# Performance work log

Hardware: AMD Instinct MI355X
Metric: run time of the kernel (lower is better)

Reference implementation:

```python
import jax, jax.numpy as jnp
import numpy as np

EPS = 1e-15

def gcn_sparse(x, row, col, ew, W, b, n):
    # PyG GCNConv: h = x@W; add self-loops (weight 1); sym-normalize; aggregate at col (target); + bias
    h = x @ W
    loop = jnp.arange(n)
    r = jnp.concatenate([row, loop])
    c = jnp.concatenate([col, loop])
    w = jnp.concatenate([ew, jnp.ones((n,), x.dtype)])
    deg = jax.ops.segment_sum(w, c, num_segments=n)
    dinv = jnp.where(deg > 0, deg ** -0.5, 0.0)
    norm = dinv[r] * w * dinv[c]
    out = jax.ops.segment_sum(norm[:, None] * h[r], c, num_segments=n)
    return out + b

def gcn_dense(x, adj, W, b):
    # Dense equivalent of dense_to_sparse + GCNConv: existing nonzero self-loops keep their
    # weight, zero-diagonal nodes get a self-loop of weight 1 (add_remaining_self_loops).
    diag = jnp.diagonal(adj)
    adj_h = adj + jnp.diag(jnp.where(diag == 0, 1.0, 0.0).astype(adj.dtype))
    deg = adj_h.sum(axis=0)  # degree at target (col) nodes
    dinv = jnp.where(deg > 0, deg ** -0.5, 0.0)
    a_norm = dinv[:, None] * adj_h * dinv[None, :]  # norm_ij = d_i^-1/2 a_ij d_j^-1/2
    return a_norm.T @ (x @ W) + b  # out_j = sum_i norm_ij h_i

def diff_pool(x, adj, s, mask=None):
    s = jax.nn.softmax(s, axis=-1)
    if mask is not None:
        x = x * mask[:, None]
        s = s * mask[:, None]
    out = s.T @ x                      # [C, F]
    out_adj = s.T @ (adj @ s)          # [C, C]
    link = jnp.linalg.norm(adj - s @ s.T) / adj.size
    ent = jnp.mean(jnp.sum(-s * jnp.log(s + EPS), axis=-1))
    return out, out_adj, link, ent

def setup_inputs() -> dict:
    N, E, F, H, C1, C2, NC = 8192, 262144, 128, 128, 1024, 128, 16
    key = jax.random.key(0)
    ks = jax.random.split(key, 16)
    x0 = jax.random.normal(ks[0], (N, F), dtype=jnp.float32)
    edge_index = jax.random.randint(ks[1], (2, E), 0, N, dtype=jnp.int32)
    edge_weight = jax.random.uniform(ks[2], (E,), dtype=jnp.float32)
    adj = jnp.zeros((N, N), jnp.float32).at[edge_index[0], edge_index[1]].add(edge_weight)
    mask = jnp.ones((N,), jnp.float32)
    g = lambda k, i, o: jax.random.normal(k, (i, o), dtype=jnp.float32) * (1.0 / np.sqrt(i))
    return {
        'x0': x0, 'edge_index': edge_index, 'edge_weight': edge_weight,
        'adj': adj, 'mask': mask,
        'W0_in': g(ks[3], F, H),      'b0_in': jnp.zeros((H,)),
        'Wp1':   g(ks[4], H, C1),     'bp1':   jnp.zeros((C1,)),
        'W1_in': g(ks[5], H, H),      'b1_in': jnp.zeros((H,)),
        'Wp2':   g(ks[6], H, C2),     'bp2':   jnp.zeros((C2,)),
        'W2_in': g(ks[7], H, H),      'b2_in': jnp.zeros((H,)),
        'W1_out': g(ks[8], 2 * H, H), 'b1_out': jnp.zeros((H,)),
        'W0_out': g(ks[9], 2 * H, NC), 'b0_out': jnp.zeros((NC,)),
    }

def reference(x0, edge_index, edge_weight, adj, mask,
              W0_in, b0_in, Wp1, bp1, W1_in, b1_in, Wp2, bp2,
              W2_in, b2_in, W1_out, b1_out, W0_out, b0_out):
    n = x0.shape[0]
    row, col = edge_index[0], edge_index[1]
    x0_ = jax.nn.relu(gcn_sparse(x0, row, col, edge_weight, W0_in, b0_in, n))
    s1 = jax.nn.relu(gcn_sparse(x0_, row, col, edge_weight, Wp1, bp1, n))
    x1, adj1, l1, e1 = diff_pool(x0_, adj, s1, mask)
    x1_ = jax.nn.relu(gcn_dense(x1, adj1, W1_in, b1_in))
    s2 = jax.nn.relu(gcn_dense(x1_, adj1, Wp2, bp2))
    x2, adj2, l2, e2 = diff_pool(x1_, adj1, s2)
    x2_out = jax.nn.relu(gcn_dense(x2, adj2, W2_in, b2_in))
    x2_out_up = s2 @ x2_out  # unpool with pre-softmax relu s2, as in source
    x1_out = jax.nn.relu(gcn_dense(jnp.concatenate([x1_, x2_out_up], axis=1), adj1, W1_out, b1_out))
    x1_out_up = s1 @ x1_out
    x0_out = jax.nn.relu(gcn_sparse(jnp.concatenate([x0_, x1_out_up], axis=1), row, col, edge_weight, W0_out, b0_out, n))
    prediction = jax.nn.log_softmax(x0_out, axis=1)
    edge_loss = l1 + e1 + l2 + e2
    return prediction, s1, edge_loss, adj1
```

## Files before the change

kernel.cpp:

```cpp
#include <hip/hip_runtime.h>
#include <math.h>


#define N_NODES 8192
#define N_EDGES 262144

typedef __attribute__((ext_vector_type(8))) short short8;
typedef __attribute__((ext_vector_type(4))) float floatx4;

#define OFF_DEG     0
#define OFF_CNTC    8192
#define OFF_CNTR    16384
#define OFF_SCAL    24576
#define ZERO_FLOATS 24592
#define OFF_COLPTR  24592
#define OFF_ROWPTR  32785
#define OFF_CURC    40978
#define OFF_CURR    49170
#define OFF_COLR    57362
#define OFF_COLN    319506
#define OFF_ROWC    581650
#define OFF_ROWW    843794
#define OFF_DINV    1105938
#define OFF_X0      1114144
#define OFF_H0      2162720
#define OFF_S       3211296
#define OFF_AN1TB   OFF_S
#define OFF_ADJ1B   (OFF_S+524288)
#define OFF_HAT     (OFF_S+1048576)
#define OFF_HBT     (OFF_S+1114112)
#define OFF_HCATT   (OFF_S+1179648)
#define OFF_S2ST    (OFF_S+1245184)
#define OFF_X0T     7405600
#define OFF_X0B     7929888
#define A2          8454176
#define OFF_X1      (A2+0)
#define OFF_Y16     (A2+131072)
#define OFF_X1_     (A2+262144)
#define OFF_S2      (A2+524288)
#define OFF_S2S     (A2+655360)
#define OFF_U       (A2+786432)
#define OFF_X2      (A2+917504)
#define OFF_ADJ2    (A2+933888)
#define OFF_HC      (A2+950272)
#define OFF_X2_     (A2+966656)
#define OFF_Z2      (A2+999424)
#define OFF_X1O     (A2+1261568)
#define OFF_P16     (A2+1392640)
#define OFF_DI1     (A2+1654784)
#define OFF_DF1     (A2+1655808)
#define OFF_DI2     (A2+1656832)
#define OFF_DF2     (A2+1656960)
#define OFF_ST      10111264
#define OFF_TBF     14305568
#define OFF_WP1T    OFF_TBF
#define OFF_PADJ    OFF_TBF
#define OFF_PG      22694176
#define OFF_PP      OFF_PG
#define OFF_PX1     31082784
#define OFF_TT2     32131360

#define OUT_PRED 0
#define OUT_S1   131072
#define OUT_LOSS 8519680
#define OUT_ADJ1 8519681

__device__ __forceinline__ unsigned short f2bf(float f) {
    union { float f; unsigned u; } v; v.f = f;
    unsigned r = (v.u + 0x7FFF + ((v.u >> 16) & 1)) >> 16;
    return (unsigned short)r;
}
__device__ __forceinline__ float bf2f(unsigned short b) {
    union { unsigned u; float f; } v; v.u = (unsigned)b << 16; return v.f;
}
__device__ __forceinline__ void gl_lds16(const unsigned short* g, unsigned short* l) {
    __builtin_amdgcn_global_load_lds(
        (const __attribute__((address_space(1))) void*)g,
        (__attribute__((address_space(3))) void*)l, 16, 0, 0);
}


__global__ void k_hist(const int* __restrict__ row, const int* __restrict__ col,
                       const float* __restrict__ ew, int E,
                       float* deg, int* cntc, int* cntr, float* sumA2) {
    __shared__ float red[256];
    int e = blockIdx.x * 256 + threadIdx.x;
    float w2 = 0.f;
    if (e < E) {
        int r = row[e], c = col[e];
        float w = ew[e];
        atomicAdd(&deg[c], w);
        atomicAdd(&cntc[c], 1);
        atomicAdd(&cntr[r], 1);
        w2 = w * w;
    }
    red[threadIdx.x] = w2; __syncthreads();
    for (int s = 128; s > 0; s >>= 1) { if (threadIdx.x < s) red[threadIdx.x] += red[threadIdx.x + s]; __syncthreads(); }
    if (threadIdx.x == 0) atomicAdd(sumA2, red[0]);
}

__global__ __launch_bounds__(1024) void k_scan(const int* cntc, const int* cntr,
        int* colptr, int* rowptr, int* curc, int* curr, int n, int E,
        const float* __restrict__ deg, float* __restrict__ dinv) {
    __shared__ int part[1024];
    int tid = threadIdx.x;
    const int per = 8;
    for (int pass = 0; pass < 2; ++pass) {
        const int* cnt = pass ? cntr : cntc;
        int* ptr = pass ? rowptr : colptr;
        int* cur = pass ? curr : curc;
        int st = tid * per;
        int loc[per]; int s = 0;
        for (int i = 0; i < per; ++i) { loc[i] = s; s += cnt[st + i]; }
        part[tid] = s; __syncthreads();
        for (int off = 1; off < 1024; off <<= 1) {
            int v = part[tid];
            int add = (tid >= off) ? part[tid - off] : 0;
            __syncthreads();
            part[tid] = v + add;
            __syncthreads();
        }
        int pre = (tid == 0) ? 0 : part[tid - 1];
        for (int i = 0; i < per; ++i) { int v = pre + loc[i]; ptr[st + i] = v; cur[st + i] = v; }
        if (tid == 0) ptr[n] = E;
        __syncthreads();
    }
    for (int i = tid; i < n; i += 1024) {
        float d = deg[i] + 1.0f;
        dinv[i] = (d > 0.f) ? 1.0f / sqrtf(d) : 0.f;
    }
}

__global__ void k_scatter(const int* __restrict__ row, const int* __restrict__ col,
                          const float* __restrict__ ew, int E, const float* __restrict__ dinv,
                          int* curc, int* curr, int* colr, float* coln, int* rowc, float* roww) {
    int e = blockIdx.x * 256 + threadIdx.x;
    if (e >= E) return;
    int r = row[e], c = col[e];
    float w = ew[e];
    float nrm = dinv[r] * w * dinv[c];
    int p = atomicAdd(&curc[c], 1);
    colr[p] = r; coln[p] = nrm;
// ... 227 lines not shown
            float a0 = As[ty * 2][kk], a1 = As[ty * 2 + 1][kk];
            float b0 = Bs[kk][tx * 2], b1 = Bs[kk][tx * 2 + 1];
            acc[0][0] += a0 * b0; acc[0][1] += a0 * b1;
            acc[1][0] += a1 * b0; acc[1][1] += a1 * b1;
        }
        __syncthreads();
    }
    if (op == 2) {
        float ss = acc[0][0] * acc[0][0] + acc[0][1] * acc[0][1]
                 + acc[1][0] * acc[1][0] + acc[1][1] * acc[1][1];
        red[tid] = ss; __syncthreads();
        for (int s = 128; s > 0; s >>= 1) { if (tid < s) red[tid] += red[tid + s]; __syncthreads(); }
        if (tid == 0) atomicAdd(ss_acc, red[0]);
        return;
    }
    float* C = (op == 0) ? C0 : C1;
    #pragma unroll
    for (int i = 0; i < 2; ++i)
        #pragma unroll
        for (int j = 0; j < 2; ++j)
            C[(size_t)(m0 + ty * 2 + i) * N + n0 + tx * 2 + j] = acc[i][j];
}

__global__ __launch_bounds__(256) void k_gemm_n16(const float* __restrict__ A, const float* __restrict__ B,
        float* __restrict__ C, int M, int K, int accum) {
    __shared__ float As[16][64];
    __shared__ float Bs[64][16];
    int tid = threadIdx.x;
    int r = tid >> 4, c = tid & 15;
    int m0 = blockIdx.x * 16;
    float acc = 0.f;
    for (int k0 = 0; k0 < K; k0 += 64) {
        #pragma unroll
        for (int l = 0; l < 4; ++l) {
            int idx = tid + 256 * l;
            int rr = idx >> 6, cc = idx & 63;
            As[rr][cc] = A[(size_t)(m0 + rr) * K + k0 + cc];
            int kk = idx >> 4, c2 = idx & 15;
            Bs[kk][c2] = B[(size_t)(k0 + kk) * 16 + c2];
        }
        __syncthreads();
        #pragma unroll 16
        for (int kk = 0; kk < 64; ++kk) acc += As[r][kk] * Bs[kk][c];
        __syncthreads();
    }
    float* p = &C[(size_t)(m0 + r) * 16 + c];
    if (accum) acc += *p;
    *p = acc;
}

__global__ __launch_bounds__(256) void k_gemm_n16_dual(
        const float* __restrict__ A0, int K0, const float* __restrict__ B0,
        const float* __restrict__ A1, int K1, const float* __restrict__ B1,
        float* __restrict__ C, int M) {
    __shared__ float As[16][64];
    __shared__ float Bs[64][16];
    int tid = threadIdx.x;
    int r = tid >> 4, c = tid & 15;
    int m0 = blockIdx.x * 16;
    float acc = 0.f;
    for (int src = 0; src < 2; ++src) {
        const float* A = src ? A1 : A0;
        const float* B = src ? B1 : B0;
        int K = src ? K1 : K0;
        for (int k0 = 0; k0 < K; k0 += 64) {
            #pragma unroll
            for (int l = 0; l < 4; ++l) {
                int idx = tid + 256 * l;
                int rr = idx >> 6, cc = idx & 63;
                As[rr][cc] = A[(size_t)(m0 + rr) * K + k0 + cc];
                int kk = idx >> 4, c2 = idx & 15;
                Bs[kk][c2] = B[(size_t)(k0 + kk) * 16 + c2];
            }
            __syncthreads();
            #pragma unroll 16
            for (int kk = 0; kk < 64; ++kk) acc += As[r][kk] * Bs[kk][c];
            __syncthreads();
        }
    }
    C[(size_t)(m0 + r) * 16 + c] = acc;
}


__global__ __launch_bounds__(256) void gemm_tn_bf16_part(
        const unsigned short* __restrict__ A, const unsigned short* __restrict__ B,
        float* __restrict__ P, int M, int N, int K) {
    __shared__ __align__(16) unsigned short As[128 * 64];
    __shared__ __align__(16) unsigned short Bs[128 * 64];
    int tid = threadIdx.x;
    int wave = tid >> 6, lane = tid & 63;
    int wm = wave >> 1, wn = wave & 1;
    int m0 = blockIdx.x * 128, n0 = blockIdx.y * 128;
    int kchunk = K / gridDim.z;
    int k0 = blockIdx.z * kchunk;
    float* Pz = P + (size_t)blockIdx.z * M * N;
    floatx4 acc[4][4] = {};
    int q = lane >> 4, lm = lane & 15;
    int lrow = lane >> 3, lcol = (lane & 7) * 8;
    for (int kt = 0; kt < kchunk; kt += 64) {
        int gk0 = k0 + kt;
        #pragma unroll
        for (int p = 0; p < 4; ++p) {
            int rbase = wave * 32 + p * 8;
            int row = rbase + lrow;
            int scol = lcol ^ ((row & 7) * 8);
            gl_lds16(&A[(size_t)(m0 + row) * K + gk0 + scol], &As[rbase * 64]);
            gl_lds16(&B[(size_t)(n0 + row) * K + gk0 + scol], &Bs[rbase * 64]);
        }
        __syncthreads();
        #pragma unroll
        for (int ks = 0; ks < 64; ks += 32) {
            short8 af[4], bf[4];
            int kk = ks + q * 8;
            #pragma unroll
            for (int i = 0; i < 4; ++i) {
                int ml = wm * 64 + i * 16 + lm;
                af[i] = *(const short8*)(&As[ml * 64 + (kk ^ ((ml & 7) * 8))]);
                int nl = wn * 64 + i * 16 + lm;
                bf[i] = *(const short8*)(&Bs[nl * 64 + (kk ^ ((nl & 7) * 8))]);
            }
            #pragma unroll
            for (int i = 0; i < 4; ++i)
                #pragma unroll
                for (int j = 0; j < 4; ++j)
                    acc[i][j] = __builtin_amdgcn_mfma_f32_16x16x32_bf16(af[i], bf[j], acc[i][j], 0, 0, 0);
        }
        __syncthreads();
    }
    for (int i = 0; i < 4; ++i) {
        int rowb = m0 + wm * 64 + i * 16 + q * 4;
        for (int j = 0; j < 4; ++j) {
            int col = n0 + wn * 64 + j * 16 + lm;
            #pragma unroll
            for (int r = 0; r < 4; ++r)
                Pz[(size_t)(rowb + r) * N + col] = acc[i][j][r];
        }
    }
}

__global__ __launch_bounds__(256) void gemm_tn_bf16_part3(
        const unsigned short* __restrict__ A,
        const unsigned short* __restrict__ B0, const unsigned short* __restrict__ B1,
        const unsigned short* __restrict__ B2,
        float* __restrict__ P0, float* __restrict__ P1, float* __restrict__ P2,
        int K) {
    __shared__ __align__(16) unsigned short As[128 * 64];
    __shared__ __align__(16) unsigned short Bs[128 * 64];
    int tid = threadIdx.x;
    int wave = tid >> 6, lane = tid & 63;
    int wm = wave >> 1, wn = wave & 1;
    int by = blockIdx.y;
    const unsigned short* B; float* P; int N, n0;
    if (by < 8)       { B = B0; P = P0; N = 1024; n0 = by * 128; }
    else if (by < 16) { B = B1; P = P1; N = 1024; n0 = (by - 8) * 128; }
    else              { B = B2; P = P2; N = 128;  n0 = 0; }
    int m0 = blockIdx.x * 128;
    int kchunk = K / gridDim.z;
    int k0 = blockIdx.z * kchunk;
    float* Pz = P + (size_t)blockIdx.z * 1024 * N;
    floatx4 acc[4][4] = {};
    int q = lane >> 4, lm = lane & 15;
    int lrow = lane >> 3, lcol = (lane & 7) * 8;
    for (int kt = 0; kt < kchunk; kt += 64) {
        int gk0 = k0 + kt;
        #pragma unroll
        for (int p = 0; p < 4; ++p) {
            int rbase = wave * 32 + p * 8;
            int row = rbase + lrow;
            int scol = lcol ^ ((row & 7) * 8);
            gl_lds16(&A[(size_t)(m0 + row) * K + gk0 + scol], &As[rbase * 64]);
            gl_lds16(&B[(size_t)(n0 + row) * K + gk0 + scol], &Bs[rbase * 64]);
        }
        __syncthreads();
        #pragma unroll
        for (int ks = 0; ks < 64; ks += 32) {
            short8 af[4], bf[4];
            int kk = ks + q * 8;
            #pragma unroll
            for (int i = 0; i < 4; ++i) {
                int ml = wm * 64 + i * 16 + lm;
                af[i] = *(const short8*)(&As[ml * 64 + (kk ^ ((ml & 7) * 8))]);
                int nl = wn * 64 + i * 16 + lm;
                bf[i] = *(const short8*)(&Bs[nl * 64 + (kk ^ ((nl & 7) * 8))]);
            }
            #pragma unroll
            for (int i = 0; i < 4; ++i)
                #pragma unroll
                for (int j = 0; j < 4; ++j)
                    acc[i][j] = __builtin_amdgcn_mfma_f32_16x16x32_bf16(af[i], bf[j], acc[i][j], 0, 0, 0);
        }
        __syncthreads();
    }
    for (int i = 0; i < 4; ++i) {
        int rowb = m0 + wm * 64 + i * 16 + q * 4;
        for (int j = 0; j < 4; ++j) {
            int col = n0 + wn * 64 + j * 16 + lm;
            #pragma unroll
            for (int r = 0; r < 4; ++r)
                Pz[(size_t)(rowb + r) * N + col] = acc[i][j][r];
        }
    }
}

__global__ __launch_bounds__(256) void gemm_tn_bf16_store(
        const unsigned short* __restrict__ A, const unsigned short* __restrict__ B,
        float* __restrict__ C, int M, int N, int K,
        const float* __restrict__ bias, int relu) {
    __shared__ __align__(16) unsigned short As[128 * 64];
    __shared__ __align__(16) unsigned short Bs[128 * 64];
    int tid = threadIdx.x;
    int wave = tid >> 6, lane = tid & 63;
    int wm = wave >> 1, wn = wave & 1;
    int m0 = blockIdx.x * 128, n0 = blockIdx.y * 128;
    floatx4 acc[4][4] = {};
    int q = lane >> 4, lm = lane & 15;
    int lrow = lane >> 3, lcol = (lane & 7) * 8;
    for (int kt = 0; kt < K; kt += 64) {
        #pragma unroll
        for (int p = 0; p < 4; ++p) {
            int rbase = wave * 32 + p * 8;
            int row = rbase + lrow;
            int scol = lcol ^ ((row & 7) * 8);
            gl_lds16(&A[(size_t)(m0 + row) * K + kt + scol], &As[rbase * 64]);
            gl_lds16(&B[(size_t)(n0 + row) * K + kt + scol], &Bs[rbase * 64]);
        }
        __syncthreads();
        #pragma unroll
        for (int ks = 0; ks < 64; ks += 32) {
            short8 af[4], bf[4];
            int kk = ks + q * 8;
            #pragma unroll
            for (int i = 0; i < 4; ++i) {
                int ml = wm * 64 + i * 16 + lm;
                af[i] = *(const short8*)(&As[ml * 64 + (kk ^ ((ml & 7) * 8))]);
                int nl = wn * 64 + i * 16 + lm;
                bf[i] = *(const short8*)(&Bs[nl * 64 + (kk ^ ((nl & 7) * 8))]);
            }
            #pragma unroll
            for (int i = 0; i < 4; ++i)
                #pragma unroll
                for (int j = 0; j < 4; ++j)
                    acc[i][j] = __builtin_amdgcn_mfma_f32_16x16x32_bf16(af[i], bf[j], acc[i][j], 0, 0, 0);
        }
        __syncthreads();
    }
    for (int i = 0; i < 4; ++i) {
        int rowb = m0 + wm * 64 + i * 16 + q * 4;
        for (int j = 0; j < 4; ++j) {
            int col = n0 + wn * 64 + j * 16 + lm;
            float bv = bias ? bias[col] : 0.f;
            #pragma unroll
            for (int r = 0; r < 4; ++r) {
                float v = acc[i][j][r] + bv;
                if (relu) v = fmaxf(v, 0.f);
                C[(size_t)(rowb + r) * N + col] = v;
            }
        }
    }
}

__global__ __launch_bounds__(256) void k_reduce3m(
        const float* __restrict__ P0, float* __restrict__ C0, unsigned short* __restrict__ Cb0, float* ss0,
        const float* __restrict__ P1, float* ss1,
        const float* __restrict__ P2, float* __restrict__ C2) {
    __shared__ float red[256];
    const float* P; float* C; unsigned short* Cb; float* ss; int n;
    if (blockIdx.y == 0)      { P = P0; C = C0;      Cb = Cb0;     ss = ss0;     n = 1024 * 1024; }
    else if (blockIdx.y == 1) { P = P1; C = nullptr; Cb = nullptr; ss = ss1;     n = 1024 * 1024; }
    else                      { P = P2; C = C2;      Cb = nullptr; ss = nullptr; n = 1024 * 128; }
    float ssv = 0.f;
    for (int i4 = (blockIdx.x * 256 + threadIdx.x) * 4; i4 < n; i4 += gridDim.x * 256 * 4) {
        float4 v = *(const float4*)(P + i4);
        #pragma unroll
        for (int s = 1; s < 8; ++s) {
            float4 w = *(const float4*)(P + (size_t)s * n + i4);
            v.x += w.x; v.y += w.y; v.z += w.z; v.w += w.w;
        }
        if (C) *(float4*)(C + i4) = v;
        if (Cb) {
            ushort4 o; o.x = f2bf(v.x); o.y = f2bf(v.y); o.z = f2bf(v.z); o.w = f2bf(v.w);
            *(ushort4*)(Cb + i4) = o;
        }
        ssv += v.x * v.x + v.y * v.y + v.z * v.z + v.w * v.w;
    }
    if (!ss) return;
    red[threadIdx.x] = ssv; __syncthreads();
    for (int s = 128; s > 0; s >>= 1) { if (threadIdx.x < s) red[threadIdx.x] += red[threadIdx.x + s]; __syncthreads(); }
    if (threadIdx.x == 0) atomicAdd(ss, red[0]);
}

__global__ __launch_bounds__(256) void k_reduce_br(const float* __restrict__ P,
        float* __restrict__ C, int n, int N, int nsplit,
        const float* __restrict__ bias, int relu) {
    for (int i4 = (blockIdx.x * 256 + threadIdx.x) * 4; i4 < n; i4 += gridDim.x * 256 * 4) {
        float4 v = *(const float4*)(P + i4);
        for (int s = 1; s < nsplit; ++s) {
            float4 w = *(const float4*)(P + (size_t)s * n + i4);
            v.x += w.x; v.y += w.y; v.z += w.z; v.w += w.w;
        }
        if (bias) {
            float4 b = *(const float4*)(bias + (i4 % N));
            v.x += b.x; v.y += b.y; v.z += b.z; v.w += b.w;
        }
        if (relu) {
            v.x = fmaxf(v.x, 0.f); v.y = fmaxf(v.y, 0.f);
            v.z = fmaxf(v.z, 0.f); v.w = fmaxf(v.w, 0.f);
        }
        *(float4*)(C + i4) = v;
    }
}


__global__ __launch_bounds__(256) void k_transpose_f2b(
        const float* __restrict__ in, unsigned short* __restrict__ outb,
        int R, int C, const float* __restrict__ rowscale) {
    __shared__ float tile[64][65];
    int rb = blockIdx.y * 64, cb = blockIdx.x * 64;
    int t = threadIdx.x;
    int lr = t >> 4, lc4 = (t & 15) * 4;
    #pragma unroll
    for (int p = 0; p < 4; ++p) {
        int r = rb + lr + p * 16;
        float4 v = *(const float4*)(in + (size_t)r * C + cb + lc4);
        float s = rowscale ? rowscale[r] : 1.0f;
        tile[lr + p * 16][lc4 + 0] = v.x * s;
        tile[lr + p * 16][lc4 + 1] = v.y * s;
        tile[lr + p * 16][lc4 + 2] = v.z * s;
        tile[lr + p * 16][lc4 + 3] = v.w * s;
    }
    __syncthreads();
    int cc0 = t >> 5, rr = (t & 31) * 2;
    #pragma unroll
    for (int p = 0; p < 8; ++p) {
        int cc = cc0 + p * 8;
        unsigned a = f2bf(tile[rr][cc]);
        unsigned b = f2bf(tile[rr + 1][cc]);
        *(unsigned*)(outb + (size_t)(cb + cc) * R + rb + rr) = a | (b << 16);
    }
}

__global__ __launch_bounds__(256) void k_transpose_b2b2(
        const unsigned short* __restrict__ in0, unsigned short* __restrict__ out0,
        const unsigned short* __restrict__ in1, unsigned short* __restrict__ out1,
        int R, int C) {
    __shared__ __align__(16) unsigned short tile[64][72];
    const unsigned short* in = blockIdx.z ? in1 : in0;
    unsigned short* out = blockIdx.z ? out1 : out0;
    int rb = blockIdx.y * 64, cb = blockIdx.x * 64;
    int t = threadIdx.x;
    int lr = t >> 3, lc = (t & 7) * 8;
    #pragma unroll
    for (int p = 0; p < 2; ++p) {
        int r = lr + p * 32;
        *(short8*)(&tile[r][lc]) = *(const short8*)(&in[(size_t)(rb + r) * C + cb + lc]);
    }
    __syncthreads();
    int cc0 = t >> 4, rr = (t & 15) * 4;
    #pragma unroll
    for (int p = 0; p < 4; ++p) {
        int cc = cc0 + p * 16;
        unsigned long long v = (unsigned long long)tile[rr][cc]
                             | ((unsigned long long)tile[rr + 1][cc] << 16)
                             | ((unsigned long long)tile[rr + 2][cc] << 32)
                             | ((unsigned long long)tile[rr + 3][cc] << 48);
        *(unsigned long long*)(&out[(size_t)(cb + cc) * R + rb + rr]) = v;
    }
}

__global__ __launch_bounds__(256) void k_anorm_tb(const float* __restrict__ adjm, int n,
        const float* __restrict__ dinvv, const float* __restrict__ dfix,
        unsigned short* __restrict__ outb) {
    __shared__ float tile[64][65];
    int rb = blockIdx.y * 64, cb = blockIdx.x * 64;
    int t = threadIdx.x;
    int lr = t >> 4, lc4 = (t & 15) * 4;
    #pragma unroll
    for (int p = 0; p < 4; ++p) {
        int i = rb + lr + p * 16;
        float4 v = *(const float4*)(adjm + (size_t)i * n + cb + lc4);
        float di = dinvv[i];
        float vv[4] = {v.x, v.y, v.z, v.w};
        #pragma unroll
        for (int q = 0; q < 4; ++q) {
            int j = cb + lc4 + q;
            float val = vv[q];
            if (i == j) val += dfix[i];
            tile[lr + p * 16][lc4 + q] = di * val * dinvv[j];
        }
    }
    __syncthreads();
    int cc0 = t >> 5, rr = (t & 31) * 2;
// ... 92 lines not shown
    m = red[0]; __syncthreads();
    float e0 = expf(v.x - m), e1 = expf(v.y - m), e2 = expf(v.z - m), e3 = expf(v.w - m);
    red[tid] = e0 + e1 + e2 + e3; __syncthreads();
    for (int s = 128; s > 0; s >>= 1) { if (tid < s) red[tid] += red[tid + s]; __syncthreads(); }
    float inv = 1.0f / red[0]; __syncthreads();
    float mk = mask ? mask[r] : 1.0f;
    float s0 = e0 * inv * mk, s1 = e1 * inv * mk, s2 = e2 * inv * mk, s3 = e3 * inv * mk;
    float ent = -(s0 * logf(s0 + 1e-15f) + s1 * logf(s1 + 1e-15f)
                + s2 * logf(s2 + 1e-15f) + s3 * logf(s3 + 1e-15f));
    ushort4 o;
    o.x = f2bf(s0); o.y = f2bf(s1); o.z = f2bf(s2); o.w = f2bf(s3);
    *(ushort4*)(Sb + (size_t)r * 1024 + tid * 4) = o;
    red[tid] = ent; __syncthreads();
    for (int s = 128; s > 0; s >>= 1) { if (tid < s) red[tid] += red[tid + s]; __syncthreads(); }
    if (tid == 0) atomicAdd(ent_acc, red[0]);
}

__global__ __launch_bounds__(256) void k_softmax_ent(const float* __restrict__ x, float* __restrict__ S,
        int W, const float* __restrict__ mask, float* ent_acc) {
    __shared__ float red[256];
    int row = blockIdx.x, tid = threadIdx.x;
    const float* xr = x + (size_t)row * W;
    float m = -3.0e38f;
    for (int q = tid; q < W; q += 256) m = fmaxf(m, xr[q]);
    red[tid] = m; __syncthreads();
    for (int s = 128; s > 0; s >>= 1) { if (tid < s) red[tid] = fmaxf(red[tid], red[tid + s]); __syncthreads(); }
    m = red[0]; __syncthreads();
    float sum = 0.f;
    for (int q = tid; q < W; q += 256) sum += expf(xr[q] - m);
    red[tid] = sum; __syncthreads();
    for (int s = 128; s > 0; s >>= 1) { if (tid < s) red[tid] += red[tid + s]; __syncthreads(); }
    float inv = 1.0f / red[0]; __syncthreads();
    float mk = mask ? mask[row] : 1.0f;
    float* Sr = S + (size_t)row * W;
    float ent = 0.f;
    for (int q = tid; q < W; q += 256) {
        float v = expf(xr[q] - m) * inv * mk;
        Sr[q] = v;
        ent -= v * logf(v + 1e-15f);
    }
    red[tid] = ent; __syncthreads();
    for (int s = 128; s > 0; s >>= 1) { if (tid < s) red[tid] += red[tid + s]; __syncthreads(); }
    if (tid == 0) atomicAdd(ent_acc, red[0]);
}

__global__ __launch_bounds__(256) void k_spmm_seg(const unsigned short* __restrict__ Sb,
        const int* __restrict__ rptr, const int* __restrict__ rowc, const float* __restrict__ roww,
        unsigned short* __restrict__ tb) {
    int wave = threadIdx.x >> 6, lane = threadIdx.x & 63;
    int r = blockIdx.x * 4 + wave;
    int j0 = blockIdx.y * 256 + lane * 4;
    const unsigned short* Sj = Sb + j0;
    float a0 = 0.f, a1 = 0.f, a2 = 0.f, a3 = 0.f;
    int e0 = rptr[r], e1 = rptr[r + 1];
    int e = e0;
    for (; e + 4 <= e1; e += 4) {
        int c0 = rowc[e], c1 = rowc[e + 1], c2 = rowc[e + 2], c3 = rowc[e + 3];
        float w0 = roww[e], w1 = roww[e + 1], w2 = roww[e + 2], w3 = roww[e + 3];
        uint2 v0 = *(const uint2*)(Sj + (size_t)c0 * 1024);
        uint2 v1 = *(const uint2*)(Sj + (size_t)c1 * 1024);
        uint2 v2 = *(const uint2*)(Sj + (size_t)c2 * 1024);
        uint2 v3 = *(const uint2*)(Sj + (size_t)c3 * 1024);
        a0 += w0 * bf2f((unsigned short)(v0.x & 0xffff)) + w1 * bf2f((unsigned short)(v1.x & 0xffff))
            + w2 * bf2f((unsigned short)(v2.x & 0xffff)) + w3 * bf2f((unsigned short)(v3.x & 0xffff));
        a1 += w0 * bf2f((unsigned short)(v0.x >> 16)) + w1 * bf2f((unsigned short)(v1.x >> 16))
            + w2 * bf2f((unsigned short)(v2.x >> 16)) + w3 * bf2f((unsigned short)(v3.x >> 16));
        a2 += w0 * bf2f((unsigned short)(v0.y & 0xffff)) + w1 * bf2f((unsigned short)(v1.y & 0xffff))
            + w2 * bf2f((unsigned short)(v2.y & 0xffff)) + w3 * bf2f((unsigned short)(v3.y & 0xffff));
        a3 += w0 * bf2f((unsigned short)(v0.y >> 16)) + w1 * bf2f((unsigned short)(v1.y >> 16))
            + w2 * bf2f((unsigned short)(v2.y >> 16)) + w3 * bf2f((unsigned short)(v3.y >> 16));
    }
    for (; e < e1; ++e) {
        int c = rowc[e]; float w = roww[e];
        uint2 v = *(const uint2*)(Sj + (size_t)c * 1024);
        a0 += w * bf2f((unsigned short)(v.x & 0xffff));
        a1 += w * bf2f((unsigned short)(v.x >> 16));
        a2 += w * bf2f((unsigned short)(v.y & 0xffff));
        a3 += w * bf2f((unsigned short)(v.y >> 16));
    }
    unsigned lo = (unsigned)f2bf(a0) | ((unsigned)f2bf(a1) << 16);
    unsigned hi = (unsigned)f2bf(a2) | ((unsigned)f2bf(a3) << 16);
    unsigned long long o = (unsigned long long)lo | ((unsigned long long)hi << 32);
    *(unsigned long long*)(tb + (size_t)r * 1024 + j0) = o;
}

__global__ __launch_bounds__(256) void k_coldfix1024(const float* __restrict__ adjm,
        float* dinvv, float* dfix, float* cross_acc) {
    __shared__ float part[4][64];
    __shared__ float red[256];
    int jl = threadIdx.x & 63;
    int j = blockIdx.x * 64 + jl;
    int rg = threadIdx.x >> 6;
    float s = 0.f;
    for (int r = rg * 256; r < rg * 256 + 256; ++r)
        s += adjm[(size_t)r * 1024 + j];
    part[rg][jl] = s;
    __syncthreads();
    float diag = 0.f;
    if (rg == 0) {
        float tot = part[0][jl] + part[1][jl] + part[2][jl] + part[3][jl];
        diag = adjm[(size_t)j * 1024 + j];
        float fix = (diag == 0.f) ? 1.0f : 0.f;
        tot += fix;
        dfix[j] = fix;
        dinvv[j] = (tot > 0.f) ? 1.0f / sqrtf(tot) : 0.f;
    }
    red[threadIdx.x] = diag; __syncthreads();
    for (int st = 128; st > 0; st >>= 1) { if (threadIdx.x < st) red[threadIdx.x] += red[threadIdx.x + st]; __syncthreads(); }
    if (threadIdx.x == 0) atomicAdd(cross_acc, red[0]);
}

__global__ __launch_bounds__(128) void k_coldfix128(const float* __restrict__ adjm,
        float* dinvv, float* dfix, float* cross2_out) {
    __shared__ float red[128];
    int j = threadIdx.x;
    float s = 0.f;
    for (int i = 0; i < 128; ++i) s += adjm[(size_t)i * 128 + j];
    float diag = adjm[(size_t)j * 128 + j];
    float fix = (diag == 0.f) ? 1.0f : 0.f;
    s += fix;
    dfix[j] = fix;
    dinvv[j] = (s > 0.f) ? 1.0f / sqrtf(s) : 0.f;
    red[j] = diag; __syncthreads();
    for (int st = 64; st > 0; st >>= 1) { if (j < st) red[j] += red[j + st]; __syncthreads(); }
    if (j == 0) *cross2_out = red[0];
}

__global__ void k_finalize(const float* __restrict__ sc, float* loss) {
    if (threadIdx.x == 0 && blockIdx.x == 0) {
        float e1     = sc[0] / 8192.0f;
        float cross  = sc[1];
        float g2     = sc[2];
        float sumA2  = sc[3];
        float ssadj1 = sc[4];
        float e2     = sc[5] / 1024.0f;
        float cross2 = sc[6];
        float g2b    = sc[7];
        float l1 = sqrtf(fmaxf(sumA2 - 2.0f * cross + g2, 0.f)) / 67108864.0f;
        float l2 = sqrtf(fmaxf(ssadj1 - 2.0f * cross2 + g2b, 0.f)) / 1048576.0f;
        *loss = l1 + e1 + l2 + e2;
    }
}


extern "C" void kernel_launch(void* const* d_in, const int* in_sizes, int n_in,
                              void* d_out, int out_size, void* d_ws, size_t ws_size,
                              hipStream_t stream) {
    const int N = N_NODES, E = N_EDGES;
    const float* x0     = (const float*)d_in[0];
    const int*   eidx   = (const int*)d_in[1];
    const float* ew     = (const float*)d_in[2];
    const float* mask   = (const float*)d_in[4];
    const float* W0_in  = (const float*)d_in[5];
    const float* b0_in  = (const float*)d_in[6];
    const float* Wp1    = (const float*)d_in[7];
    const float* bp1    = (const float*)d_in[8];
    const float* W1_in  = (const float*)d_in[9];
    const float* b1_in  = (const float*)d_in[10];
    const float* Wp2    = (const float*)d_in[11];
    const float* bp2    = (const float*)d_in[12];
    const float* W2_in  = (const float*)d_in[13];
    const float* b2_in  = (const float*)d_in[14];
    const float* W1_out = (const float*)d_in[15];
    const float* b1_out = (const float*)d_in[16];
    const float* W0_out = (const float*)d_in[17];
    const float* b0_out = (const float*)d_in[18];

    float* out   = (float*)d_out;
    float* predo = out + OUT_PRED;
    float* s1o   = out + OUT_S1;
    float* losso = out + OUT_LOSS;
    float* adj1o = out + OUT_ADJ1;

    float* wsf = (float*)d_ws;
    int*   wsi = (int*)d_ws;
    float* deg   = wsf + OFF_DEG;
    int*   cntc  = wsi + OFF_CNTC;
    int*   cntr  = wsi + OFF_CNTR;
    float* scal  = wsf + OFF_SCAL;
    int*   cptr  = wsi + OFF_COLPTR;
    int*   rptr  = wsi + OFF_ROWPTR;
    int*   curc  = wsi + OFF_CURC;
    int*   curr  = wsi + OFF_CURR;
    int*   colr  = wsi + OFF_COLR;
    float* coln  = wsf + OFF_COLN;
    int*   rowc  = wsi + OFF_ROWC;
    float* roww  = wsf + OFF_ROWW;
    float* dinv  = wsf + OFF_DINV;
    float* x0_   = wsf + OFF_X0;
    unsigned short* h0b   = (unsigned short*)(wsf + OFF_H0);
    unsigned short* Sb    = (unsigned short*)(wsf + OFF_S);
    unsigned short* TT    = (unsigned short*)(wsf + OFF_TT2);
    unsigned short* AN1TB = (unsigned short*)(wsf + OFF_AN1TB);
    unsigned short* ADJ1B = (unsigned short*)(wsf + OFF_ADJ1B);
    unsigned short* HAT   = (unsigned short*)(wsf + OFF_HAT);
    unsigned short* HBT   = (unsigned short*)(wsf + OFF_HBT);
    unsigned short* HCATT = (unsigned short*)(wsf + OFF_HCATT);
    unsigned short* S2ST  = (unsigned short*)(wsf + OFF_S2ST);
    unsigned short* ST    = (unsigned short*)(wsf + OFF_ST);
    unsigned short* TBF   = (unsigned short*)(wsf + OFF_TBF);
    unsigned short* WP1T  = (unsigned short*)(wsf + OFF_WP1T);
    unsigned short* X0T   = (unsigned short*)(wsf + OFF_X0T);
    unsigned short* x0b   = (unsigned short*)(wsf + OFF_X0B);
    float* PADJ  = wsf + OFF_PADJ;
    float* PG    = wsf + OFF_PG;
    float* PP    = wsf + OFF_PP;
    float* PX1   = wsf + OFF_PX1;
    float* x1    = wsf + OFF_X1;
    float* y16   = wsf + OFF_Y16;
    float* x1_   = wsf + OFF_X1_;
    float* s2    = wsf + OFF_S2;
    float* S2s   = wsf + OFF_S2S;
    float* u     = wsf + OFF_U;
    float* x2    = wsf + OFF_X2;
    float* adj2  = wsf + OFF_ADJ2;
    float* hC    = wsf + OFF_HC;
    float* x2_   = wsf + OFF_X2_;
    float* z2    = wsf + OFF_Z2;
    float* x1o_  = wsf + OFF_X1O;
    float* p16   = wsf + OFF_P16;
    float* di1   = wsf + OFF_DI1;
    float* df1   = wsf + OFF_DF1;
    float* di2   = wsf + OFF_DI2;
    float* df2   = wsf + OFF_DF2;

    const int* row = eidx;
    const int* col = eidx + E;

    hipMemsetAsync(wsf, 0, (size_t)ZERO_FLOATS * sizeof(float), stream);

    k_hist<<<E / 256, 256, 0, stream>>>(row, col, ew, E, deg, cntc, cntr, &scal[3]);
    k_scan<<<1, 1024, 0, stream>>>(cntc, cntr, cptr, rptr, curc, curr, N, E, deg, dinv);
    k_scatter<<<E / 256, 256, 0, stream>>>(row, col, ew, E, dinv, curc, curr, colr, coln, rowc, roww);

    gemm_ab_b16<<<dim3(2, 128), 256, 0, stream>>>(x0, W0_in, h0b, 8192, 128, 128);
    k_agg_b16<<<N, 64, 0, stream>>>(h0b, x0_, x0b, cptr, colr, coln, dinv, b0_in, 1);

    k_agg_b16<<<N, 64, 0, stream>>>(x0b, nullptr, h0b, cptr, colr, coln, dinv, nullptr, 0);
    k_transpose_f2b<<<dim3(16, 2), 256, 0, stream>>>(Wp1, WP1T, 128, 1024, nullptr);
    gemm_tn_bf16_store<<<dim3(64, 8), 256, 0, stream>>>(h0b, WP1T, s1o, 8192, 1024, 128, bp1, 1);

    k_softmax1024<<<N, 256, 0, stream>>>(s1o, Sb, mask, &scal[0]);
    k_spmm_seg<<<dim3(N / 4, 4), 256, 0, stream>>>(Sb, rptr, rowc, roww, TBF);
    k_transpose_b2b2<<<dim3(16, 128, 2), 256, 0, stream>>>(Sb, ST, TBF, TT, 8192, 1024);
    k_transpose_f2b<<<dim3(2, 128), 256, 0, stream>>>(x0_, X0T, 8192, 128, mask);

    gemm_tn_bf16_part3<<<dim3(8, 17, 8), 256, 0, stream>>>(ST, TT, ST, X0T, PADJ, PG, PX1, 8192);
    k_reduce3m<<<dim3(1024, 3), 256, 0, stream>>>(PADJ, adj1o, ADJ1B, &scal[4], PG, &scal[2], PX1, x1);

    k_coldfix1024<<<16, 256, 0, stream>>>(adj1o, di1, df1, &scal[1]);
    k_anorm_tb<<<dim3(16, 16), 256, 0, stream>>>(adj1o, 1024, di1, df1, AN1TB);

    gemm_ab32_bt<<<dim3(4, 32), 256, 0, stream>>>(x1, W1_in, HAT, 1024, 128, 128);
    gemm_tn_bf16_part<<<dim3(8, 1, 16), 256, 0, stream>>>(AN1TB, HAT, PP, 1024, 128, 1024);
    k_reduce_br<<<128, 256, 0, stream>>>(PP, x1_, 1024 * 128, 128, 16, b1_in, 1);
    gemm_ab32_bt<<<dim3(4, 32), 256, 0, stream>>>(x1_, Wp2, HBT, 1024, 128, 128);
    gemm_tn_bf16_part<<<dim3(8, 1, 16), 256, 0, stream>>>(AN1TB, HBT, PP, 1024, 128, 1024);
    k_reduce_br<<<128, 256, 0, stream>>>(PP, s2, 1024 * 128, 128, 16, bp2, 1);

    k_softmax_ent<<<1024, 256, 0, stream>>>(s2, S2s, 128, nullptr, &scal[5]);
    k_transpose_f2b<<<dim3(2, 16), 256, 0, stream>>>(S2s, S2ST, 1024, 128, nullptr);
    gemm_tn_bf16_part<<<dim3(8, 1, 16), 256, 0, stream>>>(ADJ1B, S2ST, PP, 1024, 128, 1024);
    k_reduce_br<<<128, 256, 0, stream>>>(PP, u, 1024 * 128, 128, 16, nullptr, 0);
    k_atb32_3<<<dim3(4, 4, 3), 256, 0, stream>>>(S2s, x1_, u, S2s, x2, adj2, &scal[7], 128, 128, 1024);

    k_coldfix128<<<1, 128, 0, stream>>>(adj2, di2, df2, &scal[6]);
    gemm_ab32<<<dim3(4, 4), 256, 0, stream>>>(x2, W2_in, hC, 128, 128, 128, nullptr, 0, 0);
    gemm_atb32n<<<dim3(4, 4), 256, 0, stream>>>(adj2, hC, x2_, 128, 128, 128, b2_in, di2, df2, di2);

    gemm_ab32<<<dim3(4, 4), 256, 0, stream>>>(x2_, W1_out + 128 * 128, z2, 128, 128, 128, nullptr, 0, 0);
    gemm_dual_bt<<<dim3(4, 32), 256, 0, stream>>>(x1_, W1_out, s2, z2, HCATT, 1024, 128, 128);
    gemm_tn_bf16_part<<<dim3(8, 1, 16), 256, 0, stream>>>(AN1TB, HCATT, PP, 1024, 128, 1024);
    k_reduce_br<<<128, 256, 0, stream>>>(PP, x1o_, 1024 * 128, 128, 16, b1_out, 1);

    k_gemm_n16<<<64, 256, 0, stream>>>(x1o_, W0_out + 128 * 16, y16, 1024, 128, 0);
    k_gemm_n16_dual<<<512, 256, 0, stream>>>(x0_, 128, W0_out, s1o, 1024, y16, p16, 8192);
    k_agg16_ls<<<512, 256, 0, stream>>>(p16, predo, cptr, colr, coln, dinv, b0_out);

    k_finalize<<<1, 64, 0, stream>>>(scal, losso);
}
```

Before: 945.8 us.

## Exploit S^T S symmetry, cut split-K, and drop partial-sum reductions for small GEMMs

The big pooling GEMM now computes only the upper-triangular tiles of S^T S, which is needed only for the link-loss norm, and counts off-diagonal tiles twice. Split-K drops from 8 to 4 to shrink the partial buffers. A new reduction kernel fuses the column degree, diagonal and trace computation, replacing the column-sum kernel that re-read adj1. The 1024x128 dense GEMMs switch to a non-split 64x64-tile kernel with fused bias and ReLU, which removes the 16-way partial-sum writes and the separate reduction launches. The cost is fewer blocks (32) for the small GEMMs, with a full K=1024 loop per block, and atomic accumulation for the degrees.

After: 895.2 us. -5.4%, faster.

```diff
diff --git a/kernel.cpp b/kernel.cpp
--- a/kernel.cpp
+++ b/kernel.cpp
@@ -47,6 +47,8 @@
 #define OFF_Z2      (A2+999424)
 #define OFF_X1O     (A2+1261568)
 #define OFF_P16     (A2+1392640)
+#define OFF_DEG1    OFF_P16
+#define OFF_DIAGV   (OFF_P16+1024)
 #define OFF_DI1     (A2+1654784)
 #define OFF_DF1     (A2+1655808)
 #define OFF_DI2     (A2+1656832)
@@ -54,10 +56,7 @@
 #define OFF_ST      10111264
 #define OFF_TBF     14305568
 #define OFF_WP1T    OFF_TBF
-#define OFF_PADJ    OFF_TBF
-#define OFF_PG      22694176
-#define OFF_PP      OFF_PG
-#define OFF_PX1     31082784
+#define OFF_PT      OFF_TBF
 #define OFF_TT2     32131360
 
 #define OUT_PRED 0
@@ -451,18 +450,27 @@
 }
 
 
-__global__ __launch_bounds__(256) void gemm_tn_bf16_part(
-        const unsigned short* __restrict__ A, const unsigned short* __restrict__ B,
-        float* __restrict__ P, int M, int N, int K) {
+__global__ __launch_bounds__(256) void gemm_tn_bf16_tiles(
+        const unsigned short* __restrict__ ST_,
+        const unsigned short* __restrict__ TT_,
+        const unsigned short* __restrict__ X0T_,
+        float* __restrict__ P, int K) {
     __shared__ __align__(16) unsigned short As[128 * 64];
     __shared__ __align__(16) unsigned short Bs[128 * 64];
     int tid = threadIdx.x;
     int wave = tid >> 6, lane = tid & 63;
     int wm = wave >> 1, wn = wave & 1;
-    int m0 = blockIdx.x * 128, n0 = blockIdx.y * 128;
-    int kchunk = K / gridDim.z;
-    int k0 = blockIdx.z * kchunk;
-    float* Pz = P + (size_t)blockIdx.z * M * N;
+    int tile = blockIdx.x;
+    int m, n; const unsigned short* B;
+    if (tile < 64)       { m = tile >> 3; n = tile & 7; B = TT_; }
+    else if (tile < 100) { int p = tile - 64; int ti = 0;
+                           while (p >= 8 - ti) { p -= 8 - ti; ++ti; }
+                           m = ti; n = ti + p; B = ST_; }
+    else                 { m = tile - 100; n = 0; B = X0T_; }
+    int m0 = m * 128, n0 = n * 128;
+    int kchunk = K / gridDim.y;
+    int k0 = blockIdx.y * kchunk;
+    float* Pz = P + ((size_t)blockIdx.y * 108 + tile) * 16384;
     floatx4 acc[4][4] = {};
     int q = lane >> 4, lm = lane & 15;
     int lrow = lane >> 3, lcol = (lane & 7) * 8;
@@ -473,7 +481,7 @@
             int rbase = wave * 32 + p * 8;
             int row = rbase + lrow;
             int scol = lcol ^ ((row & 7) * 8);
-            gl_lds16(&A[(size_t)(m0 + row) * K + gk0 + scol], &As[rbase * 64]);
+            gl_lds16(&ST_[(size_t)(m0 + row) * K + gk0 + scol], &As[rbase * 64]);
             gl_lds16(&B[(size_t)(n0 + row) * K + gk0 + scol], &Bs[rbase * 64]);
         }
         __syncthreads();
@@ -497,76 +505,146 @@
         __syncthreads();
     }
     for (int i = 0; i < 4; ++i) {
-        int rowb = m0 + wm * 64 + i * 16 + q * 4;
+        int lr = wm * 64 + i * 16 + q * 4;
         for (int j = 0; j < 4; ++j) {
-            int col = n0 + wn * 64 + j * 16 + lm;
+            int lc = wn * 64 + j * 16 + lm;
             #pragma unroll
             for (int r = 0; r < 4; ++r)
-                Pz[(size_t)(rowb + r) * N + col] = acc[i][j][r];
-        }
-    }
-}
-
-__global__ __launch_bounds__(256) void gemm_tn_bf16_part3(
-        const unsigned short* __restrict__ A,
-        const unsigned short* __restrict__ B0, const unsigned short* __restrict__ B1,
-        const unsigned short* __restrict__ B2,
-        float* __restrict__ P0, float* __restrict__ P1, float* __restrict__ P2,
-        int K) {
-    __shared__ __align__(16) unsigned short As[128 * 64];
-    __shared__ __align__(16) unsigned short Bs[128 * 64];
-    int tid = threadIdx.x;
-    int wave = tid >> 6, lane = tid & 63;
-    int wm = wave >> 1, wn = wave & 1;
-    int by = blockIdx.y;
-    const unsigned short* B; float* P; int N, n0;
-    if (by < 8)       { B = B0; P = P0; N = 1024; n0 = by * 128; }
-    else if (by < 16) { B = B1; P = P1; N = 1024; n0 = (by - 8) * 128; }
-    else              { B = B2; P = P2; N = 128;  n0 = 0; }
-    int m0 = blockIdx.x * 128;
-    int kchunk = K / gridDim.z;
-    int k0 = blockIdx.z * kchunk;
-    float* Pz = P + (size_t)blockIdx.z * 1024 * N;
-    floatx4 acc[4][4] = {};
+                Pz[(size_t)(lr + r) * 128 + lc] = acc[i][j][r];
+        }
+    }
+}
+
+__global__ __launch_bounds__(256) void k_reduce_tiles(
+        const float* __restrict__ P,
+        float* __restrict__ adj1o, unsigned short* __restrict__ adj1b,
+        float* __restrict__ x1, float* __restrict__ deg1, float* __restrict__ diagv,
+        float* __restrict__ scal) {
+    __shared__ float colsum[128];
+    __shared__ float red[256];
+    int tile = blockIdx.y, half = blockIdx.x, tid = threadIdx.x;
+    if (tid < 128) colsum[tid] = 0.f;
+    __syncthreads();
+    int m, n, kind;
+    if (tile < 64)       { kind = 0; m = tile >> 3; n = tile & 7; }
+    else if (tile < 100) { kind = 1; int p = tile - 64; int ti = 0;
+                           while (p >= 8 - ti) { p -= 8 - ti; ++ti; }
+                           m = ti; n = ti + p; }
+    else                 { kind = 2; m = tile - 100; n = 0; }
+    const float* Pt = P + (size_t)tile * 16384 + half * 8192;
+    const size_t zstr = (size_t)108 * 16384;
+    float ss = 0.f, tr = 0.f;
+    float cs0 = 0.f, cs1 = 0.f, cs2 = 0.f, cs3 = 0.f;
+    int cc = (tid * 4) & 127;
+    bool diagTile = (kind == 0) && (m == n);
+    float wgt = (kind == 1 && m != n) ? 2.f : 1.f;
+    for (int it = 0; it < 8; ++it) {
+        int i4 = tid * 4 + it * 1024;
+        float4 v = *(const float4*)(Pt + i4);
+        #pragma unroll
+        for (int z = 1; z < 4; ++z) {
+            float4 w4 = *(const float4*)(Pt + zstr * z + i4);
+            v.x += w4.x; v.y += w4.y; v.z += w4.z; v.w += w4.w;
+        }
+        int rr = i4 >> 7;
+        if (kind == 0) {
+            size_t gaddr = (size_t)(m * 128 + half * 64 + rr) * 1024 + n * 128 + cc;
+            *(float4*)(adj1o + gaddr) = v;
+            ushort4 o; o.x = f2bf(v.x); o.y = f2bf(v.y); o.z = f2bf(v.z); o.w = f2bf(v.w);
+            *(ushort4*)(adj1b + gaddr) = o;
+            cs0 += v.x; cs1 += v.y; cs2 += v.z; cs3 += v.w;
+            ss += v.x * v.x + v.y * v.y + v.z * v.z + v.w * v.w;
+            if (diagTile) {
+                int dloc = half * 64 + rr;
+                int dj = dloc - cc;
+                if (dj >= 0 && dj < 4) {
+                    float dv = (dj == 0) ? v.x : (dj == 1) ? v.y : (dj == 2) ? v.z : v.w;
+                    diagv[m * 128 + dloc] = dv;
+                    tr += dv;
+                }
+            }
+        } else if (kind == 1) {
+            ss += wgt * (v.x * v.x + v.y * v.y + v.z * v.z + v.w * v.w);
+        } else {
+            *(float4*)(x1 + (size_t)(m * 128 + half * 64) * 128 + i4) = v;
+        }
+    }
+    if (kind == 2) return;
+    if (kind == 0) {
+        atomicAdd(&colsum[cc + 0], cs0);
+        atomicAdd(&colsum[cc + 1], cs1);
+        atomicAdd(&colsum[cc + 2], cs2);
+        atomicAdd(&colsum[cc + 3], cs3);
+    }
+    __syncthreads();
+    if (kind == 0 && tid < 128)
+        atomicAdd(&deg1[n * 128 + tid], colsum[tid]);
+    red[tid] = ss; __syncthreads();
+    for (int s = 128; s > 0; s >>= 1) { if (tid < s) red[tid] += red[tid + s]; __syncthreads(); }
+    if (tid == 0) atomicAdd((kind == 0) ? &scal[4] : &scal[2], red[0]);
+    if (diagTile) {
+        __syncthreads();
+        red[tid] = tr; __syncthreads();
+        for (int s = 128; s > 0; s >>= 1) { if (tid < s) red[tid] += red[tid + s]; __syncthreads(); }
+        if (tid == 0) atomicAdd(&scal[1], red[0]);
+    }
+}
+
+__global__ __launch_bounds__(1024) void k_dinv1024(const float* __restrict__ deg1,
+        const float* __restrict__ diagv, float* __restrict__ di, float* __restrict__ df) {
+    int j = threadIdx.x;
+    float s = deg1[j];
+    float fix = (diagv[j] == 0.f) ? 1.0f : 0.f;
+    s += fix;
+    df[j] = fix;
+    di[j] = (s > 0.f) ? 1.0f / sqrtf(s) : 0.f;
+}
+
+__global__ __launch_bounds__(256) void gemm_tn_bf16_n128(
+        const unsigned short* __restrict__ A, const unsigned short* __restrict__ B,
+        float* __restrict__ C, int K,
+        const float* __restrict__ bias, int relu) {
+    __shared__ __align__(16) unsigned short As[64 * 64];
+    __shared__ __align__(16) unsigned short Bs[64 * 64];
+    int tid = threadIdx.x, wave = tid >> 6, lane = tid & 63;
+    int m0 = blockIdx.x * 64, n0 = blockIdx.y * 64;
+    floatx4 acc[4] = {};
     int q = lane >> 4, lm = lane & 15;
     int lrow = lane >> 3, lcol = (lane & 7) * 8;
-    for (int kt = 0; kt < kchunk; kt += 64) {
-        int gk0 = k0 + kt;
-        #pragma unroll
-        for (int p = 0; p < 4; ++p) {
-            int rbase = wave * 32 + p * 8;
+    for (int kt = 0; kt < K; kt += 64) {
+        #pragma unroll
+        for (int p = 0; p < 2; ++p) {
+            int rbase = wave * 16 + p * 8;
             int row = rbase + lrow;
             int scol = lcol ^ ((row & 7) * 8);
-            gl_lds16(&A[(size_t)(m0 + row) * K + gk0 + scol], &As[rbase * 64]);
-            gl_lds16(&B[(size_t)(n0 + row) * K + gk0 + scol], &Bs[rbase * 64]);
+            gl_lds16(&A[(size_t)(m0 + row) * K + kt + scol], &As[rbase * 64]);
+            gl_lds16(&B[(size_t)(n0 + row) * K + kt + scol], &Bs[rbase * 64]);
         }
         __syncthreads();
         #pragma unroll
         for (int ks = 0; ks < 64; ks += 32) {
-            short8 af[4], bf[4];
             int kk = ks + q * 8;
-            #pragma unroll
-            for (int i = 0; i < 4; ++i) {
-                int ml = wm * 64 + i * 16 + lm;
-                af[i] = *(const short8*)(&As[ml * 64 + (kk ^ ((ml & 7) * 8))]);
-                int nl = wn * 64 + i * 16 + lm;
-                bf[i] = *(const short8*)(&Bs[nl * 64 + (kk ^ ((nl & 7) * 8))]);
+            int ml = wave * 16 + lm;
+            short8 af = *(const short8*)(&As[ml * 64 + (kk ^ ((ml & 7) * 8))]);
+            #pragma unroll
+            for (int j = 0; j < 4; ++j) {
+                int nl = j * 16 + lm;
+                short8 bf = *(const short8*)(&Bs[nl * 64 + (kk ^ ((nl & 7) * 8))]);
+                acc[j] = __builtin_amdgcn_mfma_f32_16x16x32_bf16(af, bf, acc[j], 0, 0, 0);
             }
-            #pragma unroll
-            for (int i = 0; i < 4; ++i)
-                #pragma unroll
-                for (int j = 0; j < 4; ++j)
-                    acc[i][j] = __builtin_amdgcn_mfma_f32_16x16x32_bf16(af[i], bf[j], acc[i][j], 0, 0, 0);
-        }
-        __syncthreads();
-    }
-    for (int i = 0; i < 4; ++i) {
-        int rowb = m0 + wm * 64 + i * 16 + q * 4;
-        for (int j = 0; j < 4; ++j) {
-            int col = n0 + wn * 64 + j * 16 + lm;
-            #pragma unroll
-            for (int r = 0; r < 4; ++r)
-                Pz[(size_t)(rowb + r) * N + col] = acc[i][j][r];
+        }
+        __syncthreads();
+    }
+    #pragma unroll
+    for (int j = 0; j < 4; ++j) {
+        int col = n0 + j * 16 + lm;
+        float bv = bias ? bias[col] : 0.f;
+        int rowb = m0 + wave * 16 + q * 4;
+        #pragma unroll
+        for (int r = 0; r < 4; ++r) {
+            float v = acc[j][r] + bv;
+            if (relu) v = fmaxf(v, 0.f);
+            C[(size_t)(rowb + r) * 128 + col] = v;
         }
     }
 }
@@ -625,57 +703,6 @@
                 C[(size_t)(rowb + r) * N + col] = v;
             }
         }
-    }
-}
-
-__global__ __launch_bounds__(256) void k_reduce3m(
-        const float* __restrict__ P0, float* __restrict__ C0, unsigned short* __restrict__ Cb0, float* ss0,
-        const float* __restrict__ P1, float* ss1,
-        const float* __restrict__ P2, float* __restrict__ C2) {
-    __shared__ float red[256];
-    const float* P; float* C; unsigned short* Cb; float* ss; int n;
-    if (blockIdx.y == 0)      { P = P0; C = C0;      Cb = Cb0;     ss = ss0;     n = 1024 * 1024; }
-    else if (blockIdx.y == 1) { P = P1; C = nullptr; Cb = nullptr; ss = ss1;     n = 1024 * 1024; }
-    else                      { P = P2; C = C2;      Cb = nullptr; ss = nullptr; n = 1024 * 128; }
-    float ssv = 0.f;
-    for (int i4 = (blockIdx.x * 256 + threadIdx.x) * 4; i4 < n; i4 += gridDim.x * 256 * 4) {
-        float4 v = *(const float4*)(P + i4);
-        #pragma unroll
-        for (int s = 1; s < 8; ++s) {
-            float4 w = *(const float4*)(P + (size_t)s * n + i4);
-            v.x += w.x; v.y += w.y; v.z += w.z; v.w += w.w;
-        }
-        if (C) *(float4*)(C + i4) = v;
-        if (Cb) {
-            ushort4 o; o.x = f2bf(v.x); o.y = f2bf(v.y); o.z = f2bf(v.z); o.w = f2bf(v.w);
-            *(ushort4*)(Cb + i4) = o;
-        }
-        ssv += v.x * v.x + v.y * v.y + v.z * v.z + v.w * v.w;
-    }
-    if (!ss) return;
-    red[threadIdx.x] = ssv; __syncthreads();
-    for (int s = 128; s > 0; s >>= 1) { if (threadIdx.x < s) red[threadIdx.x] += red[threadIdx.x + s]; __syncthreads(); }
-    if (threadIdx.x == 0) atomicAdd(ss, red[0]);
-}
-
-__global__ __launch_bounds__(256) void k_reduce_br(const float* __restrict__ P,
-        float* __restrict__ C, int n, int N, int nsplit,
-        const float* __restrict__ bias, int relu) {
-    for (int i4 = (blockIdx.x * 256 + threadIdx.x) * 4; i4 < n; i4 += gridDim.x * 256 * 4) {
-        float4 v = *(const float4*)(P + i4);
-        for (int s = 1; s < nsplit; ++s) {
-            float4 w = *(const float4*)(P + (size_t)s * n + i4);
-            v.x += w.x; v.y += w.y; v.z += w.z; v.w += w.w;
-        }
-        if (bias) {
-            float4 b = *(const float4*)(bias + (i4 % N));
-            v.x += b.x; v.y += b.y; v.z += b.z; v.w += b.w;
-        }
-        if (relu) {
-            v.x = fmaxf(v.x, 0.f); v.y = fmaxf(v.y, 0.f);
-            v.z = fmaxf(v.z, 0.f); v.w = fmaxf(v.w, 0.f);
-        }
-        *(float4*)(C + i4) = v;
     }
 }
 
@@ -934,32 +961,6 @@
     unsigned hi = (unsigned)f2bf(a2) | ((unsigned)f2bf(a3) << 16);
     unsigned long long o = (unsigned long long)lo | ((unsigned long long)hi << 32);
     *(unsigned long long*)(tb + (size_t)r * 1024 + j0) = o;
-}
-
-__global__ __launch_bounds__(256) void k_coldfix1024(const float* __restrict__ adjm,
-        float* dinvv, float* dfix, float* cross_acc) {
-    __shared__ float part[4][64];
-    __shared__ float red[256];
-    int jl = threadIdx.x & 63;
-    int j = blockIdx.x * 64 + jl;
-    int rg = threadIdx.x >> 6;
-    float s = 0.f;
-    for (int r = rg * 256; r < rg * 256 + 256; ++r)
-        s += adjm[(size_t)r * 1024 + j];
-    part[rg][jl] = s;
-    __syncthreads();
-    float diag = 0.f;
-    if (rg == 0) {
-        float tot = part[0][jl] + part[1][jl] + part[2][jl] + part[3][jl];
-        diag = adjm[(size_t)j * 1024 + j];
-        float fix = (diag == 0.f) ? 1.0f : 0.f;
-        tot += fix;
-        dfix[j] = fix;
-        dinvv[j] = (tot > 0.f) ? 1.0f / sqrtf(tot) : 0.f;
-    }
-    red[threadIdx.x] = diag; __syncthreads();
-    for (int st = 128; st > 0; st >>= 1) { if (threadIdx.x < st) red[threadIdx.x] += red[threadIdx.x + st]; __syncthreads(); }
-    if (threadIdx.x == 0) atomicAdd(cross_acc, red[0]);
 }
 
 __global__ __launch_bounds__(128) void k_coldfix128(const float* __restrict__ adjm,
@@ -1054,10 +1055,7 @@
     unsigned short* WP1T  = (unsigned short*)(wsf + OFF_WP1T);
     unsigned short* X0T   = (unsigned short*)(wsf + OFF_X0T);
     unsigned short* x0b   = (unsigned short*)(wsf + OFF_X0B);
-    float* PADJ  = wsf + OFF_PADJ;
-    float* PG    = wsf + OFF_PG;
-    float* PP    = wsf + OFF_PP;
-    float* PX1   = wsf + OFF_PX1;
+    float* PT    = wsf + OFF_PT;
     float* x1    = wsf + OFF_X1;
     float* y16   = wsf + OFF_Y16;
     float* x1_   = wsf + OFF_X1_;
@@ -1071,6 +1069,8 @@
     float* z2    = wsf + OFF_Z2;
     float* x1o_  = wsf + OFF_X1O;
     float* p16   = wsf + OFF_P16;
+    float* deg1  = wsf + OFF_DEG1;
+    float* diagv = wsf + OFF_DIAGV;
     float* di1   = wsf + OFF_DI1;
     float* df1   = wsf + OFF_DF1;
     float* di2   = wsf + OFF_DI2;
@@ -1080,6 +1080,7 @@
     const int* col = eidx + E;
 
     hipMemsetAsync(wsf, 0, (size_t)ZERO_FLOATS * sizeof(float), stream);
+    hipMemsetAsync(deg1, 0, 1024 * sizeof(float), stream);
 
     k_hist<<<E / 256, 256, 0, stream>>>(row, col, ew, E, deg, cntc, cntr, &scal[3]);
     k_scan<<<1, 1024, 0, stream>>>(cntc, cntr, cptr, rptr, curc, curr, N, E, deg, dinv);
@@ -1097,23 +1098,19 @@
     k_transpose_b2b2<<<dim3(16, 128, 2), 256, 0, stream>>>(Sb, ST, TBF, TT, 8192, 1024);
     k_transpose_f2b<<<dim3(2, 128), 256, 0, stream>>>(x0_, X0T, 8192, 128, mask);
 
-    gemm_tn_bf16_part3<<<dim3(8, 17, 8), 256, 0, stream>>>(ST, TT, ST, X0T, PADJ, PG, PX1, 8192);
-    k_reduce3m<<<dim3(1024, 3), 256, 0, stream>>>(PADJ, adj1o, ADJ1B, &scal[4], PG, &scal[2], PX1, x1);
-
-    k_coldfix1024<<<16, 256, 0, stream>>>(adj1o, di1, df1, &scal[1]);
+    gemm_tn_bf16_tiles<<<dim3(108, 4), 256, 0, stream>>>(ST, TT, X0T, PT, 8192);
+    k_reduce_tiles<<<dim3(2, 108), 256, 0, stream>>>(PT, adj1o, ADJ1B, x1, deg1, diagv, scal);
+    k_dinv1024<<<1, 1024, 0, stream>>>(deg1, diagv, di1, df1);
     k_anorm_tb<<<dim3(16, 16), 256, 0, stream>>>(adj1o, 1024, di1, df1, AN1TB);
 
     gemm_ab32_bt<<<dim3(4, 32), 256, 0, stream>>>(x1, W1_in, HAT, 1024, 128, 128);
-    gemm_tn_bf16_part<<<dim3(8, 1, 16), 256, 0, stream>>>(AN1TB, HAT, PP, 1024, 128, 1024);
-    k_reduce_br<<<128, 256, 0, stream>>>(PP, x1_, 1024 * 128, 128, 16, b1_in, 1);
+    gemm_tn_bf16_n128<<<dim3(16, 2), 256, 0, stream>>>(AN1TB, HAT, x1_, 1024, b1_in, 1);
     gemm_ab32_bt<<<dim3(4, 32), 256, 0, stream>>>(x1_, Wp2, HBT, 1024, 128, 128);
-    gemm_tn_bf16_part<<<dim3(8, 1, 16), 256, 0, stream>>>(AN1TB, HBT, PP, 1024, 128, 1024);
-    k_reduce_br<<<128, 256, 0, stream>>>(PP, s2, 1024 * 128, 128, 16, bp2, 1);
+    gemm_tn_bf16_n128<<<dim3(16, 2), 256, 0, stream>>>(AN1TB, HBT, s2, 1024, bp2, 1);
 
     k_softmax_ent<<<1024, 256, 0, stream>>>(s2, S2s, 128, nullptr, &scal[5]);
     k_transpose_f2b<<<dim3(2, 16), 256, 0, stream>>>(S2s, S2ST, 1024, 128, nullptr);
-    gemm_tn_bf16_part<<<dim3(8, 1, 16), 256, 0, stream>>>(ADJ1B, S2ST, PP, 1024, 128, 1024);
-    k_reduce_br<<<128, 256, 0, stream>>>(PP, u, 1024 * 128, 128, 16, nullptr, 0);
+    gemm_tn_bf16_n128<<<dim3(16, 2), 256, 0, stream>>>(ADJ1B, S2ST, u, 1024, nullptr, 0);
     k_atb32_3<<<dim3(4, 4, 3), 256, 0, stream>>>(S2s, x1_, u, S2s, x2, adj2, &scal[7], 128, 128, 1024);
 
     k_coldfix128<<<1, 128, 0, stream>>>(adj2, di2, df2, &scal[6]);
@@ -1122,8 +1119,7 @@
 
     gemm_ab32<<<dim3(4, 4), 256, 0, stream>>>(x2_, W1_out + 128 * 128, z2, 128, 128, 128, nullptr, 0, 0);
     gemm_dual_bt<<<dim3(4, 32), 256, 0, stream>>>(x1_, W1_out, s2, z2, HCATT, 1024, 128, 128);
-    gemm_tn_bf16_part<<<dim3(8, 1, 16), 256, 0, stream>>>(AN1TB, HCATT, PP, 1024, 128, 1024);
-    k_reduce_br<<<128, 256, 0, stream>>>(PP, x1o_, 1024 * 128, 128, 16, b1_out, 1);
+    gemm_tn_bf16_n128<<<dim3(16, 2), 256, 0, stream>>>(AN1TB, HCATT, x1o_, 1024, b1_out, 1);
 
     k_gemm_n16<<<64, 256, 0, stream>>>(x1o_, W0_out + 128 * 16, y16, 1024, 128, 0);
     k_gemm_n16_dual<<<512, 256, 0, stream>>>(x0_, 128, W0_out, s1o, 1024, y16, p16, 8192);
```
